# Optimization experiments

Hardware: AMD Instinct MI355X
Metric: run time of the kernel (lower is better)

The kernel has to match this reference:

```python
import jax, jax.numpy as jnp
import numpy as np

NEG_SLOPE = 0.2  # PyG GATConv default
EPS = 1e-16      # PyG softmax denominator guard


def setup_inputs() -> dict:
    key = jax.random.key(0)
    k1, k2, k3, k4, k5 = jax.random.split(key, 5)
    N, E, D_in, H, C = 100000, 1600000, 128, 4, 32
    x = jax.random.normal(k1, (N, D_in), dtype=jnp.float32)
    edge_index = jax.random.randint(k2, (2, E), 0, N, dtype=jnp.int64)
    W = jax.random.normal(k3, (D_in, H * C), dtype=jnp.float32) * 0.05
    att_src = jax.random.normal(k4, (H, C), dtype=jnp.float32) * 0.05
    att_dst = jax.random.normal(k5, (H, C), dtype=jnp.float32) * 0.05
    bias = jnp.zeros((H * C,), dtype=jnp.float32)
    return {"x": x, "edge_index": edge_index, "W": W,
            "att_src": att_src, "att_dst": att_dst, "bias": bias}


def reference(x, edge_index, W, att_src, att_dst, bias):
    N = x.shape[0]
    H, C = att_src.shape
    # add self-loops (PyG default add_self_loops=True)
    loop = jnp.arange(N, dtype=edge_index.dtype)
    src = jnp.concatenate([edge_index[0], loop])  # [E+N]
    dst = jnp.concatenate([edge_index[1], loop])  # [E+N]

    # linear projection per head: [N, H, C]
    h = (x @ W).reshape(N, H, C)
    # per-node attention logits: [N, H]
    a_src = jnp.einsum('nhc,hc->nh', h, att_src)
    a_dst = jnp.einsum('nhc,hc->nh', h, att_dst)

    # per-edge logits with LeakyReLU: [E+N, H]
    e = jax.nn.leaky_relu(a_src[src] + a_dst[dst], NEG_SLOPE)

    # segment softmax over incoming edges of each dst node
    m = jax.ops.segment_max(e, dst, num_segments=N)          # [N, H]
    m = jnp.where(jnp.isfinite(m), m, 0.0)                    # empty segments
    ex = jnp.exp(e - m[dst])                                  # [E+N, H]
    s = jax.ops.segment_sum(ex, dst, num_segments=N)          # [N, H]
    alpha = ex / (s[dst] + EPS)                               # [E+N, H]

    # weighted message aggregation: [N, H, C]
    msgs = h[src] * alpha[:, :, None]
    out = jax.ops.segment_sum(msgs, dst, num_segments=N)

    # concat heads (attention_concat=True) + bias
    return out.reshape(N, H * C) + bias
```

## Files before the change

kernel.cpp:

```cpp
#include <hip/hip_runtime.h>

#define HC 128
#define NHEAD 4
#define HDIM 32
#define NEG 0.2f
#define GEPS 1e-16f
#define BSH 9
#define TILE 2048
#define CAP 8960

__device__ __forceinline__ unsigned int bf16rn(float f) {
  unsigned int u = __float_as_uint(f);
  return (u + 0x7fffu + ((u >> 16) & 1u)) >> 16;
}

__global__ __launch_bounds__(256) void k_mega(const float* __restrict__ x,
                                              const float* __restrict__ W,
                                              const float* __restrict__ att_src,
                                              const float* __restrict__ att_dst,
                                              unsigned int* __restrict__ hb,
                                              float2* __restrict__ easrc,
                                              float2* __restrict__ eadst,
                                              const int* __restrict__ src,
                                              const int* __restrict__ dst,
                                              int* __restrict__ bcur0,
                                              unsigned int* __restrict__ ebuf,
                                              int N, int E, int PB, int nbuck) {
  __shared__ union SM {
    float xs[64][68];
    struct {
      unsigned int stage[TILE];
      unsigned char bkt[TILE];
      int hist[256], loff[256], lcur[256], gbase[256], ss[256];
    } p;
  } sm;

  if ((int)blockIdx.x >= PB) {
    int t = threadIdx.x;
    int e0 = ((int)blockIdx.x - PB) * TILE;
    int cnt = min(TILE, E - e0);
    sm.p.hist[t] = 0;
    __syncthreads();
    for (int i = t; i < cnt; i += 256)
      atomicAdd(&sm.p.hist[dst[e0 + i] >> BSH], 1);
    __syncthreads();
    int v = sm.p.hist[t];
    int xx = v;
    sm.p.ss[t] = xx;
    __syncthreads();
    for (int off = 1; off < 256; off <<= 1) {
      int y = (t >= off) ? sm.p.ss[t - off] : 0;
      __syncthreads();
      xx += y;
      sm.p.ss[t] = xx;
      __syncthreads();
    }
    sm.p.loff[t] = xx - v;
    sm.p.lcur[t] = xx - v;
    __syncthreads();
    for (int i = t; i < cnt; i += 256) {
      int d = dst[e0 + i];
      int s = src[e0 + i];
      int b = d >> BSH;
      int r = atomicAdd(&sm.p.lcur[b], 1);
      sm.p.stage[r] = ((unsigned int)s << BSH) | (unsigned int)(d & ((1 << BSH) - 1));
      sm.p.bkt[r] = (unsigned char)b;
    }
    __syncthreads();
    if (t < nbuck) {
      int c = sm.p.lcur[t] - sm.p.loff[t];
      sm.p.gbase[t] = t * CAP + (c ? atomicAdd(&bcur0[t], c) : 0);
    }
    __syncthreads();
    for (int i = t; i < cnt; i += 256) {
      int b = sm.p.bkt[i];
      ebuf[sm.p.gbase[b] + (i - sm.p.loff[b])] = sm.p.stage[i];
    }
    return;
  }

  int row0 = blockIdx.x * 64;
  const int tr = (threadIdx.x >> 4) << 2;
  const int c0 = (threadIdx.x & 15) << 3;
  float acc[4][8];
#pragma unroll
  for (int i = 0; i < 4; ++i)
#pragma unroll
    for (int j = 0; j < 8; ++j) acc[i][j] = 0.f;

  for (int kb = 0; kb < 128; kb += 64) {
    if (kb) __syncthreads();
    for (int i = threadIdx.x; i < 1024; i += 256) {
      int r = i >> 4;
      int cc = (i & 15) << 2;
      float4 v = make_float4(0.f, 0.f, 0.f, 0.f);
      int row = row0 + r;
      if (row < N) v = *(const float4*)(x + (size_t)row * HC + kb + cc);
      *(float4*)&sm.xs[r][cc] = v;
    }
    __syncthreads();
    for (int k = 0; k < 64; ++k) {
      const float4 w0 = *(const float4*)(W + (size_t)(kb + k) * HC + c0);
      const float4 w1 = *(const float4*)(W + (size_t)(kb + k) * HC + c0 + 4);
      float wv[8] = {w0.x, w0.y, w0.z, w0.w, w1.x, w1.y, w1.z, w1.w};
      float xv[4] = {sm.xs[tr][k], sm.xs[tr + 1][k], sm.xs[tr + 2][k], sm.xs[tr + 3][k]};
#pragma unroll
      for (int i = 0; i < 4; ++i)
#pragma unroll
        for (int j = 0; j < 8; ++j) acc[i][j] += xv[i] * wv[j];
    }
  }
#pragma unroll
  for (int i = 0; i < 4; ++i) {
    int row = row0 + tr + i;
    if (row < N) {
      uint4 p;
      p.x = bf16rn(acc[i][0]) | (bf16rn(acc[i][1]) << 16);
      p.y = bf16rn(acc[i][2]) | (bf16rn(acc[i][3]) << 16);
      p.z = bf16rn(acc[i][4]) | (bf16rn(acc[i][5]) << 16);
      p.w = bf16rn(acc[i][6]) | (bf16rn(acc[i][7]) << 16);
      *(uint4*)(hb + (size_t)row * 64 + (c0 >> 1)) = p;
    }
  }
  int head = (threadIdx.x & 15) >> 2;
  int cc = c0 & 31;
  const float4 s0 = *(const float4*)(att_src + head * HDIM + cc);
  const float4 s1 = *(const float4*)(att_src + head * HDIM + cc + 4);
  const float4 d0 = *(const float4*)(att_dst + head * HDIM + cc);
  const float4 d1 = *(const float4*)(att_dst + head * HDIM + cc + 4);
  float asv[4], adv[4];
#pragma unroll
  for (int i = 0; i < 4; ++i) {
    asv[i] = acc[i][0] * s0.x + acc[i][1] * s0.y + acc[i][2] * s0.z + acc[i][3] * s0.w +
             acc[i][4] * s1.x + acc[i][5] * s1.y + acc[i][6] * s1.z + acc[i][7] * s1.w;
    adv[i] = acc[i][0] * d0.x + acc[i][1] * d0.y + acc[i][2] * d0.z + acc[i][3] * d0.w +
             acc[i][4] * d1.x + acc[i][5] * d1.y + acc[i][6] * d1.z + acc[i][7] * d1.w;
  }
#pragma unroll
  for (int off = 1; off < 4; off <<= 1) {
#pragma unroll
    for (int i = 0; i < 4; ++i) {
      asv[i] += __shfl_xor(asv[i], off);
      adv[i] += __shfl_xor(adv[i], off);
    }
  }
  if ((threadIdx.x & 3) == 0) {
#pragma unroll
    for (int i = 0; i < 4; ++i) {
      int row = row0 + tr + i;
      if (row < N) {
        easrc[row * NHEAD + head] = make_float2(__expf(asv[i]), __expf(NEG * asv[i]));
        eadst[row * NHEAD + head] = make_float2(__expf(adv[i]), __expf(NEG * adv[i]));
      }
    }
  }
}

__global__ __launch_bounds__(1024) void k_partB(const unsigned int* __restrict__ ebuf,
                                                const int* __restrict__ bcur0,
                                                int* __restrict__ rowptr,
                                                int* __restrict__ rowend,
                                                int* __restrict__ srcidx, int N) {
  __shared__ unsigned int se[CAP];
  __shared__ int lcnt[512], ss[512];
  int b = blockIdx.x;
  int t = threadIdx.x;
  int beg = b * CAP;
  int cnt = bcur0[b];
  if (t < 512) lcnt[t] = 0;
  __syncthreads();
  for (int j = t; j < cnt; j += 1024) {
    unsigned int v = ebuf[beg + j];
    se[j] = v;
    atomicAdd(&lcnt[v & 511], 1);
  }
  __syncthreads();
  int v = 0, x = 0;
  if (t < 512) {
    v = lcnt[t];
    x = v;
    ss[t] = x;
  }
  __syncthreads();
  for (int off = 1; off < 512; off <<= 1) {
    int y = (t >= off && t < 512) ? ss[t - off] : 0;
    __syncthreads();
    if (t < 512) {
      x += y;
      ss[t] = x;
    }
    __syncthreads();
  }
  int ex = x - v;
  if (t < 512) {
    int node = (b << BSH) + t;
    if (node < N) {
      rowptr[node] = beg + ex;
      rowend[node] = beg + x;
    }
  }
  __syncthreads();
  if (t < 512) lcnt[t] = ex;
  if (t < 16) srcidx[beg + cnt + t] = 0;
  __syncthreads();
  for (int j = t; j < cnt; j += 1024) {
    unsigned int v2 = se[j];
    int pos = beg + atomicAdd(&lcnt[v2 & 511], 1);
    srcidx[pos] = (int)((v2 >> BSH) << 8);
  }
}

#define CONS(uu, ff)                                               \
  {                                                                \
    float ex = fmaxf((ff).x * edx, (ff).y * edy);                  \
    acc0 = fmaf(__uint_as_float((uu).x << 16), ex, acc0);          \
    acc1 = fmaf(__uint_as_float((uu).x & 0xffff0000u), ex, acc1);  \
    acc2 = fmaf(__uint_as_float((uu).y << 16), ex, acc2);          \
    acc3 = fmaf(__uint_as_float((uu).y & 0xffff0000u), ex, acc3);  \
    ssum += ex;                                                    \
  }
#define GATHER(U, F, O)                                            \
  U##0 = *(const uint2*)(hbp + O##0);                              \
  U##1 = *(const uint2*)(hbp + O##1);                              \
  U##2 = *(const uint2*)(hbp + O##2);                              \
  U##3 = *(const uint2*)(hbp + O##3);                              \
  F##0 = *(const float2*)(eap + (O##0 >> 3));                      \
  F##1 = *(const float2*)(eap + (O##1 >> 3));                      \
  F##2 = *(const float2*)(eap + (O##2 >> 3));                      \
  F##3 = *(const float2*)(eap + (O##3 >> 3));

__global__ __launch_bounds__(256) void k_agg(const int* __restrict__ rowptr,
                                             const int* __restrict__ rowend,
                                             const int* __restrict__ srcoff,
                                             const unsigned int* __restrict__ hb,
                                             const float2* __restrict__ easrc,
                                             const float2* __restrict__ eadst,
                                             const float* __restrict__ bias,
                                             float* __restrict__ out, int N) {
  int n = blockIdx.x * 8 + (threadIdx.x >> 5);
  if (n >= N) return;
  int lane = threadIdx.x & 31;
  int head = lane >> 3;
  const char* hbp = (const char*)hb + (lane << 3);
  const char* eap = (const char*)easrc + (head << 3);
  float2 ed = eadst[n * NHEAD + head];
  float edx = ed.x, edy = ed.y;
  float2 es_own = *(const float2*)(eap + ((size_t)n << 5));
  float exs = fmaxf(es_own.x * edx, es_own.y * edy);
  uint2 us = *(const uint2*)(hbp + ((size_t)n << 8));
  float acc0 = __uint_as_float(us.x << 16) * exs;
  float acc1 = __uint_as_float(us.x & 0xffff0000u) * exs;
  float acc2 = __uint_as_float(us.y << 16) * exs;
  float acc3 = __uint_as_float(us.y & 0xffff0000u) * exs;
  float ssum = exs;

  int beg = rowptr[n], end = rowend[n];
  int rem = end - beg;
  int Q = rem >> 2;
  const int* sp = srcoff + beg;
  if (Q) {
    int oA0 = sp[0], oA1 = sp[1], oA2 = sp[2], oA3 = sp[3];
    int oB0 = 0, oB1 = 0, oB2 = 0, oB3 = 0;
    uint2 uA0, uA1, uA2, uA3, uB0, uB1, uB2, uB3;
    float2 fA0, fA1, fA2, fA3, fB0, fB1, fB2, fB3;
    GATHER(uA, fA, oA)
    if (Q >= 2) { oB0 = sp[4]; oB1 = sp[5]; oB2 = sp[6]; oB3 = sp[7]; }
    while (Q >= 2) {
      GATHER(uB, fB, oB)
      oA0 = sp[8]; oA1 = sp[9]; oA2 = sp[10]; oA3 = sp[11];
      CONS(uA0, fA0) CONS(uA1, fA1) CONS(uA2, fA2) CONS(uA3, fA3)
      GATHER(uA, fA, oA)
      oB0 = sp[12]; oB1 = sp[13]; oB2 = sp[14]; oB3 = sp[15];
      CONS(uB0, fB0) CONS(uB1, fB1) CONS(uB2, fB2) CONS(uB3, fB3)
      sp += 8;
      Q -= 2;
    }
    if (Q == 1) { CONS(uA0, fA0) CONS(uA1, fA1) CONS(uA2, fA2) CONS(uA3, fA3) }
  }
  int tail = rem & 3;
  const int* tp = srcoff + beg + (rem & ~3);
  while (tail-- > 0) {
    int o = *tp++;
    uint2 uu = *(const uint2*)(hbp + o);
    float2 ff = *(const float2*)(eap + (o >> 3));
    CONS(uu, ff)
  }
  float inv = 1.0f / (ssum + GEPS);
  const float4 bv = *(const float4*)(bias + lane * 4);
  *(float4*)(out + (size_t)n * HC + lane * 4) =
      make_float4(fmaf(acc0, inv, bv.x), fmaf(acc1, inv, bv.y),
                  fmaf(acc2, inv, bv.z), fmaf(acc3, inv, bv.w));
}

extern "C" void kernel_launch(void* const* d_in, const int* in_sizes, int n_in,
                              void* d_out, int out_size, void* d_ws, size_t ws_size,
                              hipStream_t stream) {
  const float* x       = (const float*)d_in[0];
  const int*   ei      = (const int*)d_in[1];
  const float* W       = (const float*)d_in[2];
  const float* att_src = (const float*)d_in[3];
  const float* att_dst = (const float*)d_in[4];
  const float* bias    = (const float*)d_in[5];
  float* out = (float*)d_out;

  const int N = in_sizes[0] / HC;
  const int E = in_sizes[1] / 2;
  const int* src = ei;
  const int* dst = ei + E;
  const int nbuck = (N + (1 << BSH) - 1) >> BSH;
  const int PB = (N + 63) / 64;
  const int AB = (E + TILE - 1) / TILE;

  unsigned int* hb = (unsigned int*)d_ws;
  float2* easrc = (float2*)(hb + (size_t)N * 64);
  float2* eadst = easrc + (size_t)N * NHEAD;
  int* rowptr = (int*)(eadst + (size_t)N * NHEAD);
  int* rowend = rowptr + N;
  int* srcidx = rowend + N;
  unsigned int* ebuf = (unsigned int*)(srcidx + (size_t)nbuck * CAP + 16);
  int* bcur0 = (int*)(ebuf + (size_t)nbuck * CAP);

  hipMemsetAsync(bcur0, 0, 256 * sizeof(int), stream);
  k_mega<<<PB + AB, 256, 0, stream>>>(x, W, att_src, att_dst, hb, easrc, eadst,
                                      src, dst, bcur0, ebuf, N, E, PB, nbuck);
  k_partB<<<nbuck, 1024, 0, stream>>>(ebuf, bcur0, rowptr, rowend, srcidx, N);
  k_agg<<<(N + 7) / 8, 256, 0, stream>>>(rowptr, rowend, srcidx, hb, easrc, eadst, bias, out, N);
}
```

Measured before the change: 274.4 us.

## Fuse bucket CSR build into aggregation kernel using shared-memory edge lists

Merges the per-bucket counting-sort kernel and the aggregation kernel into one kernel. Each 1024-thread block rebuilds the bucket's row offsets and keeps the source list for its half of the bucket's nodes in LDS, then aggregates 256 nodes in 8 rounds of 32 warps-of-32. This removes the global rowptr/rowend/srcidx writes and reads and one launch. In exchange, each bucket's edge buffer is scanned twice (once per half-block), grid parallelism drops to 2 blocks per bucket, and large LDS use limits occupancy, which may hurt latency hiding in the gather loop.

```diff
diff --git a/kernel.cpp b/kernel.cpp
--- a/kernel.cpp
+++ b/kernel.cpp
@@ -156,60 +156,6 @@
   }
 }
 
-__global__ __launch_bounds__(1024) void k_partB(const unsigned int* __restrict__ ebuf,
-                                                const int* __restrict__ bcur0,
-                                                int* __restrict__ rowptr,
-                                                int* __restrict__ rowend,
-                                                int* __restrict__ srcidx, int N) {
-  __shared__ unsigned int se[CAP];
-  __shared__ int lcnt[512], ss[512];
-  int b = blockIdx.x;
-  int t = threadIdx.x;
-  int beg = b * CAP;
-  int cnt = bcur0[b];
-  if (t < 512) lcnt[t] = 0;
-  __syncthreads();
-  for (int j = t; j < cnt; j += 1024) {
-    unsigned int v = ebuf[beg + j];
-    se[j] = v;
-    atomicAdd(&lcnt[v & 511], 1);
-  }
-  __syncthreads();
-  int v = 0, x = 0;
-  if (t < 512) {
-    v = lcnt[t];
-    x = v;
-    ss[t] = x;
-  }
-  __syncthreads();
-  for (int off = 1; off < 512; off <<= 1) {
-    int y = (t >= off && t < 512) ? ss[t - off] : 0;
-    __syncthreads();
-    if (t < 512) {
-      x += y;
-      ss[t] = x;
-    }
-    __syncthreads();
-  }
-  int ex = x - v;
-  if (t < 512) {
-    int node = (b << BSH) + t;
-    if (node < N) {
-      rowptr[node] = beg + ex;
-      rowend[node] = beg + x;
-    }
-  }
-  __syncthreads();
-  if (t < 512) lcnt[t] = ex;
-  if (t < 16) srcidx[beg + cnt + t] = 0;
-  __syncthreads();
-  for (int j = t; j < cnt; j += 1024) {
-    unsigned int v2 = se[j];
-    int pos = beg + atomicAdd(&lcnt[v2 & 511], 1);
-    srcidx[pos] = (int)((v2 >> BSH) << 8);
-  }
-}
-
 #define CONS(uu, ff)                                               \
   {                                                                \
     float ex = fmaxf((ff).x * edx, (ff).y * edy);                  \
@@ -229,67 +175,118 @@
   F##2 = *(const float2*)(eap + (O##2 >> 3));                      \
   F##3 = *(const float2*)(eap + (O##3 >> 3));
 
-__global__ __launch_bounds__(256) void k_agg(const int* __restrict__ rowptr,
-                                             const int* __restrict__ rowend,
-                                             const int* __restrict__ srcoff,
-                                             const unsigned int* __restrict__ hb,
-                                             const float2* __restrict__ easrc,
-                                             const float2* __restrict__ eadst,
-                                             const float* __restrict__ bias,
-                                             float* __restrict__ out, int N) {
-  int n = blockIdx.x * 8 + (threadIdx.x >> 5);
-  if (n >= N) return;
-  int lane = threadIdx.x & 31;
-  int head = lane >> 3;
+__global__ __launch_bounds__(1024) void k_fused(const unsigned int* __restrict__ ebuf,
+                                                const int* __restrict__ bcur0,
+                                                const unsigned int* __restrict__ hb,
+                                                const float2* __restrict__ easrc,
+                                                const float2* __restrict__ eadst,
+                                                const float* __restrict__ bias,
+                                                float* __restrict__ out, int N) {
+  __shared__ int srcl[CAP + 8];
+  __shared__ int lcnt[512], ss[512], rowb[513];
+  const int b = blockIdx.x >> 1;
+  const int half = blockIdx.x & 1;
+  const int t = threadIdx.x;
+  const int beg = b * CAP;
+  const int cnt = bcur0[b];
+
+  const int g = t >> 5;
+  const int lane = t & 31;
+  const int head = lane >> 3;
   const char* hbp = (const char*)hb + (lane << 3);
   const char* eap = (const char*)easrc + (head << 3);
-  float2 ed = eadst[n * NHEAD + head];
-  float edx = ed.x, edy = ed.y;
-  float2 es_own = *(const float2*)(eap + ((size_t)n << 5));
-  float exs = fmaxf(es_own.x * edx, es_own.y * edy);
-  uint2 us = *(const uint2*)(hbp + ((size_t)n << 8));
-  float acc0 = __uint_as_float(us.x << 16) * exs;
-  float acc1 = __uint_as_float(us.x & 0xffff0000u) * exs;
-  float acc2 = __uint_as_float(us.y << 16) * exs;
-  float acc3 = __uint_as_float(us.y & 0xffff0000u) * exs;
-  float ssum = exs;
-
-  int beg = rowptr[n], end = rowend[n];
-  int rem = end - beg;
-  int Q = rem >> 2;
-  const int* sp = srcoff + beg;
-  if (Q) {
-    int oA0 = sp[0], oA1 = sp[1], oA2 = sp[2], oA3 = sp[3];
-    int oB0 = 0, oB1 = 0, oB2 = 0, oB3 = 0;
-    uint2 uA0, uA1, uA2, uA3, uB0, uB1, uB2, uB3;
-    float2 fA0, fA1, fA2, fA3, fB0, fB1, fB2, fB3;
-    GATHER(uA, fA, oA)
-    if (Q >= 2) { oB0 = sp[4]; oB1 = sp[5]; oB2 = sp[6]; oB3 = sp[7]; }
-    while (Q >= 2) {
-      GATHER(uB, fB, oB)
-      oA0 = sp[8]; oA1 = sp[9]; oA2 = sp[10]; oA3 = sp[11];
-      CONS(uA0, fA0) CONS(uA1, fA1) CONS(uA2, fA2) CONS(uA3, fA3)
+
+  int node0 = (b << BSH) + (half << 8) + g;
+  float2 edP = eadst[node0 * NHEAD + head];
+  float2 esP = *(const float2*)(eap + ((size_t)node0 << 5));
+  uint2 usP = *(const uint2*)(hbp + ((size_t)node0 << 8));
+
+  if (t < 512) lcnt[t] = 0;
+  __syncthreads();
+  for (int j = t; j < cnt; j += 1024)
+    atomicAdd(&lcnt[ebuf[beg + j] & 511], 1);
+  __syncthreads();
+  int v = 0, x = 0;
+  if (t < 512) { v = lcnt[t]; x = v; ss[t] = x; }
+  __syncthreads();
+  for (int off = 1; off < 512; off <<= 1) {
+    int y = (t >= off && t < 512) ? ss[t - off] : 0;
+    __syncthreads();
+    if (t < 512) { x += y; ss[t] = x; }
+    __syncthreads();
+  }
+  if (t < 512) { rowb[t] = x - v; lcnt[t] = x - v; }
+  if (t == 511) rowb[512] = x;
+  __syncthreads();
+  if (t < 8) srcl[rowb[(half + 1) << 8] + t] = 0;
+  for (int j = t; j < cnt; j += 1024) {
+    unsigned int v2 = ebuf[beg + j];
+    int nl = v2 & 511;
+    if ((nl >> 8) == half) {
+      int pos = atomicAdd(&lcnt[nl], 1);
+      srcl[pos] = (int)((v2 >> BSH) << 8);
+    }
+  }
+  __syncthreads();
+
+  for (int r = 0; r < 8; ++r) {
+    float2 ed = edP, es_own = esP;
+    uint2 us = usP;
+    if (r < 7) {
+      int nn = (b << BSH) + (half << 8) + (r + 1) * 32 + g;
+      edP = eadst[nn * NHEAD + head];
+      esP = *(const float2*)(eap + ((size_t)nn << 5));
+      usP = *(const uint2*)(hbp + ((size_t)nn << 8));
+    }
+    int idx = (half << 8) + r * 32 + g;
+    int node = (b << BSH) + idx;
+    float edx = ed.x, edy = ed.y;
+    float exs = fmaxf(es_own.x * edx, es_own.y * edy);
+    float acc0 = __uint_as_float(us.x << 16) * exs;
+    float acc1 = __uint_as_float(us.x & 0xffff0000u) * exs;
+    float acc2 = __uint_as_float(us.y << 16) * exs;
+    float acc3 = __uint_as_float(us.y & 0xffff0000u) * exs;
+    float ssum = exs;
+
+    int sb = rowb[idx];
+    int rem = rowb[idx + 1] - sb;
+    int Q = rem >> 2;
+    if (Q) {
+      int oA0 = srcl[sb + 0], oA1 = srcl[sb + 1], oA2 = srcl[sb + 2], oA3 = srcl[sb + 3];
+      int oB0 = 0, oB1 = 0, oB2 = 0, oB3 = 0;
+      uint2 uA0, uA1, uA2, uA3, uB0, uB1, uB2, uB3;
+      float2 fA0, fA1, fA2, fA3, fB0, fB1, fB2, fB3;
       GATHER(uA, fA, oA)
-      oB0 = sp[12]; oB1 = sp[13]; oB2 = sp[14]; oB3 = sp[15];
-      CONS(uB0, fB0) CONS(uB1, fB1) CONS(uB2, fB2) CONS(uB3, fB3)
-      sp += 8;
-      Q -= 2;
-    }
-    if (Q == 1) { CONS(uA0, fA0) CONS(uA1, fA1) CONS(uA2, fA2) CONS(uA3, fA3) }
-  }
-  int tail = rem & 3;
-  const int* tp = srcoff + beg + (rem & ~3);
-  while (tail-- > 0) {
-    int o = *tp++;
-    uint2 uu = *(const uint2*)(hbp + o);
-    float2 ff = *(const float2*)(eap + (o >> 3));
-    CONS(uu, ff)
-  }
-  float inv = 1.0f / (ssum + GEPS);
-  const float4 bv = *(const float4*)(bias + lane * 4);
-  *(float4*)(out + (size_t)n * HC + lane * 4) =
-      make_float4(fmaf(acc0, inv, bv.x), fmaf(acc1, inv, bv.y),
-                  fmaf(acc2, inv, bv.z), fmaf(acc3, inv, bv.w));
+      if (Q >= 2) { oB0 = srcl[sb + 4]; oB1 = srcl[sb + 5]; oB2 = srcl[sb + 6]; oB3 = srcl[sb + 7]; }
+      while (Q >= 2) {
+        GATHER(uB, fB, oB)
+        oA0 = srcl[sb + 8]; oA1 = srcl[sb + 9]; oA2 = srcl[sb + 10]; oA3 = srcl[sb + 11];
+        CONS(uA0, fA0) CONS(uA1, fA1) CONS(uA2, fA2) CONS(uA3, fA3)
+        GATHER(uA, fA, oA)
+        oB0 = srcl[sb + 12]; oB1 = srcl[sb + 13]; oB2 = srcl[sb + 14]; oB3 = srcl[sb + 15];
+        CONS(uB0, fB0) CONS(uB1, fB1) CONS(uB2, fB2) CONS(uB3, fB3)
+        sb += 8;
+        Q -= 2;
+      }
+      if (Q == 1) { CONS(uA0, fA0) CONS(uA1, fA1) CONS(uA2, fA2) CONS(uA3, fA3) sb += 4; }
+      else sb += 4;
+    }
+    int tb = rowb[idx] + (rem & ~3);
+    int tail = rem & 3;
+    while (tail-- > 0) {
+      int o = srcl[tb++];
+      uint2 uu = *(const uint2*)(hbp + o);
+      float2 ff = *(const float2*)(eap + (o >> 3));
+      CONS(uu, ff)
+    }
+    if (node < N) {
+      float inv = 1.0f / (ssum + GEPS);
+      const float4 bv = *(const float4*)(bias + lane * 4);
+      *(float4*)(out + (size_t)node * HC + lane * 4) =
+          make_float4(fmaf(acc0, inv, bv.x), fmaf(acc1, inv, bv.y),
+                      fmaf(acc2, inv, bv.z), fmaf(acc3, inv, bv.w));
+    }
+  }
 }
 
 extern "C" void kernel_launch(void* const* d_in, const int* in_sizes, int n_in,
@@ -314,15 +311,11 @@
   unsigned int* hb = (unsigned int*)d_ws;
   float2* easrc = (float2*)(hb + (size_t)N * 64);
   float2* eadst = easrc + (size_t)N * NHEAD;
-  int* rowptr = (int*)(eadst + (size_t)N * NHEAD);
-  int* rowend = rowptr + N;
-  int* srcidx = rowend + N;
-  unsigned int* ebuf = (unsigned int*)(srcidx + (size_t)nbuck * CAP + 16);
+  unsigned int* ebuf = (unsigned int*)(eadst + (size_t)N * NHEAD);
   int* bcur0 = (int*)(ebuf + (size_t)nbuck * CAP);
 
   hipMemsetAsync(bcur0, 0, 256 * sizeof(int), stream);
   k_mega<<<PB + AB, 256, 0, stream>>>(x, W, att_src, att_dst, hb, easrc, eadst,
                                       src, dst, bcur0, ebuf, N, E, PB, nbuck);
-  k_partB<<<nbuck, 1024, 0, stream>>>(ebuf, bcur0, rowptr, rowend, srcidx, N);
-  k_agg<<<(N + 7) / 8, 256, 0, stream>>>(rowptr, rowend, srcidx, hb, easrc, eadst, bias, out, N);
+  k_fused<<<nbuck * 2, 1024, 0, stream>>>(ebuf, bcur0, hb, easrc, eadst, bias, out, N);
 }
```

After: 287.0 us. 1.05x slower.
